# Optimization experiments

Hardware: AMD Instinct MI355X
Metric: run time of the kernel (lower is better)

The kernel has to match this reference:

```python
import jax, jax.numpy as jnp
import numpy as np

N, F, HID, H, B = 400000, 128, 32, 4, 2000

def setup_inputs() -> dict:
    key = jax.random.key(0)
    ks = jax.random.split(key, 8)
    atom_fea = jax.random.normal(ks[0], (N, F), dtype=jnp.float32)
    segment_ids = jnp.sort(jax.random.randint(ks[1], (N,), 0, B, dtype=jnp.int32))
    s = 0.05
    return {
        "atom_fea": atom_fea,
        "segment_ids": segment_ids,
        "num_crystals": B,
        "W1": jax.random.normal(ks[2], (F, HID), dtype=jnp.float32) * s,
        "b1": jnp.zeros((HID,), dtype=jnp.float32),
        "W2": jax.random.normal(ks[3], (HID, H), dtype=jnp.float32) * s,
        "b2": jnp.zeros((H,), dtype=jnp.float32),
        "Wp": jax.random.normal(ks[4], (H * F, F), dtype=jnp.float32) * s,
        "bp": jnp.zeros((F,), dtype=jnp.float32),
    }

def reference(atom_fea, segment_ids, num_crystals, W1, b1, W2, b2, Wp, bp):
    # key MLP: (N,F) -> (N,H) attention logits (dropout is eval no-op)
    logits = jax.nn.silu(atom_fea @ W1 + b1) @ W2 + b2  # (N,H)
    # segment softmax over atoms within each crystal, per head
    seg_max = jax.ops.segment_max(logits, segment_ids, num_segments=num_crystals)
    ex = jnp.exp(logits - seg_max[segment_ids])
    denom = jax.ops.segment_sum(ex, segment_ids, num_segments=num_crystals)
    w = ex / denom[segment_ids]  # (N,H)
    # per-head softmax-weighted segment sum of atom features -> (B,H,F)
    weighted = jax.ops.segment_sum(
        w[:, :, None] * atom_fea[:, None, :], segment_ids, num_segments=num_crystals
    )
    flat = weighted.reshape(num_crystals, -1)  # (B, H*F)
    return jax.nn.silu(flat @ Wp + bp)  # (B,F)
```

## Files before the change

### kernel.cpp

```cpp
#include <hip/hip_runtime.h>
#include <math.h>

#define F 128
#define HID 32
#define NH 4
#define WTILE 16
#define BTILE 64
#define ROWB 512
#define PJC 4

typedef __attribute__((ext_vector_type(8))) short bf16x8;
typedef __attribute__((ext_vector_type(4))) float f32x4;

__device__ __forceinline__ float silu_f(float x) {
    return x / (1.0f + __expf(-x));
}

__device__ __forceinline__ uint f2bf(float f) {
    union { float f; uint u; } v; v.f = f;
    uint r = v.u + 0x7fffu + ((v.u >> 16) & 1u);
    return r >> 16;
}

__device__ __forceinline__ uint cvtpk_bf16(float lo, float hi) {
    uint r;
    asm("v_cvt_pk_bf16_f32 %0, %1, %2" : "=v"(r) : "v"(lo), "v"(hi));
    return r;
}

__device__ __forceinline__ void gload_lds16(const void* g, void* l) {
    __builtin_amdgcn_global_load_lds(
        (const __attribute__((address_space(1))) void*)g,
        (__attribute__((address_space(3))) void*)l, 16, 0, 0);
}

__global__ void seg_starts_kernel(const int* __restrict__ seg, int* __restrict__ starts,
                                  int N, int B) {
    int i = blockIdx.x * blockDim.x + threadIdx.x;
    if (i >= N) return;
    int id = seg[i];
    if (i == 0) {
        for (int b = 0; b <= id; ++b) starts[b] = 0;
    } else {
        int prev = seg[i - 1];
        for (int b = prev + 1; b <= id; ++b) starts[b] = i;
    }
    if (i == N - 1) {
        for (int b = id + 1; b <= B; ++b) starts[b] = N;
    }
}

__global__ __launch_bounds__(256, 2) void fused11_kernel(
    const float* __restrict__ atom_fea, const int* __restrict__ starts,
    const float* __restrict__ W1, const float* __restrict__ b1,
    const float* __restrict__ W2, const float* __restrict__ b2,
    float* __restrict__ gWacc) {
    __shared__ float sBuf[NH][2][WTILE * F];
    __shared__ float sTW[NH][WTILE * NH];

    const int t = threadIdx.x;
    const int b = blockIdx.x;
    const int start = starts[b];
    const int end = starts[b + 1];
    const int wv = t >> 6;
    const int lane = t & 63;
    const int lg = lane >> 4;
    const int l15 = lane & 15;
    const int ch = lane & 3;
    const int co = lane >> 2;
    const int lrh = lane >> 5;
    const int lch = lane & 31;

    bf16x8 w1f[2][4];
    #pragma unroll
    for (int m0 = 0; m0 < 2; ++m0)
        #pragma unroll
        for (int kk = 0; kk < 4; ++kk) {
            bf16x8 fr;
            #pragma unroll
            for (int j = 0; j < 8; ++j)
                fr[j] = (short)f2bf(W1[(kk * 32 + lg * 8 + j) * HID + m0 * 16 + l15]);
            w1f[m0][kk] = fr;
        }
    float b1r[8], w2r[8][4];
    #pragma unroll
    for (int m0 = 0; m0 < 2; ++m0)
        #pragma unroll
        for (int r = 0; r < 4; ++r) {
            const int h = m0 * 16 + lg * 4 + r;
            b1r[m0 * 4 + r] = b1[h];
            #pragma unroll
            for (int j = 0; j < 4; ++j) w2r[m0 * 4 + r][j] = W2[h * NH + j];
        }
    const float b2r0 = b2[0], b2r1 = b2[1], b2r2 = b2[2], b2r3 = b2[3];

    float m0_ = -INFINITY, m1_ = -INFINITY, m2_ = -INFINITY, m3_ = -INFINITY;
    float s0_ = 0.0f, s1_ = 0.0f, s2_ = 0.0f, s3_ = 0.0f;
    float acc8[8] = {0, 0, 0, 0, 0, 0, 0, 0};

    const int nt = (end > start) ? (end - start + BTILE - 1) / BTILE : 0;
    const char* gb = (const char*)atom_fea;
    char* bufA = (char*)&sBuf[wv][0][0];
    char* bufB = (char*)&sBuf[wv][1][0];

    if (nt > 0) {
        #pragma unroll
        for (int i = 0; i < 8; ++i) {
            const int lr = 2 * i + lrh;
            int ga = start + wv * WTILE + lr; ga = (ga < end) ? ga : end - 1;
            gload_lds16(gb + (size_t)ga * ROWB + ((lch ^ (lr & 7)) << 4), bufA + i * 1024);
        }
    }
    asm volatile("s_waitcnt vmcnt(0)" ::: "memory");

    int pb = 0;
    for (int ti = 0; ti < nt; ++ti) {
        const int base = start + ti * BTILE;
        const int T = min(BTILE, end - base);
        const int Tw = min(T - wv * WTILE, WTILE);
        char* bufc = pb ? bufB : bufA;

        if (ti + 1 < nt) {
            char* bufn = pb ? bufA : bufB;
            const int nb = base + BTILE;
            #pragma unroll
            for (int i = 0; i < 8; ++i) {
                const int lr = 2 * i + lrh;
                int ga = nb + wv * WTILE + lr; ga = (ga < end) ? ga : end - 1;
                gload_lds16(gb + (size_t)ga * ROWB + ((lch ^ (lr & 7)) << 4), bufn + i * 1024);
            }
        }

        if (Tw > 0) {
            f32x4 a0, a1;
            #pragma unroll
            for (int r = 0; r < 4; ++r) { a0[r] = b1r[r]; a1[r] = b1r[4 + r]; }
            const char* rb = bufc + l15 * ROWB;
            const int rs = l15 & 7;
            #pragma unroll
            for (int kk = 0; kk < 4; ++kk) {
                const int c0 = kk * 8 + lg * 2;
                const float4 va = *(const float4*)(rb + ((c0 ^ rs) << 4));
                const float4 vb = *(const float4*)(rb + (((c0 + 1) ^ rs) << 4));
                union { bf16x8 v; uint u[4]; } fr;
                fr.u[0] = cvtpk_bf16(va.x, va.y);
                fr.u[1] = cvtpk_bf16(va.z, va.w);
                fr.u[2] = cvtpk_bf16(vb.x, vb.y);
                fr.u[3] = cvtpk_bf16(vb.z, vb.w);
                a0 = __builtin_amdgcn_mfma_f32_16x16x32_bf16(w1f[0][kk], fr.v, a0, 0, 0, 0);
                a1 = __builtin_amdgcn_mfma_f32_16x16x32_bf16(w1f[1][kk], fr.v, a1, 0, 0, 0);
            }
            float p0 = 0, p1 = 0, p2 = 0, p3 = 0;
            #pragma unroll
            for (int r = 0; r < 4; ++r) {
                const float sa = silu_f(a0[r]);
                const float sb = silu_f(a1[r]);
                p0 = fmaf(sa, w2r[r][0], fmaf(sb, w2r[4 + r][0], p0));
                p1 = fmaf(sa, w2r[r][1], fmaf(sb, w2r[4 + r][1], p1));
                p2 = fmaf(sa, w2r[r][2], fmaf(sb, w2r[4 + r][2], p2));
                p3 = fmaf(sa, w2r[r][3], fmaf(sb, w2r[4 + r][3], p3));
            }
            p0 += __shfl_xor(p0, 16); p0 += __shfl_xor(p0, 32);
            p1 += __shfl_xor(p1, 16); p1 += __shfl_xor(p1, 32);
            p2 += __shfl_xor(p2, 16); p2 += __shfl_xor(p2, 32);
            p3 += __shfl_xor(p3, 16); p3 += __shfl_xor(p3, 32);
            const bool valid = (l15 < Tw);
            const float v0 = valid ? p0 + b2r0 : -INFINITY;
            const float v1 = valid ? p1 + b2r1 : -INFINITY;
            const float v2 = valid ? p2 + b2r2 : -INFINITY;
            const float v3 = valid ? p3 + b2r3 : -INFINITY;

            const float dm = fmaxf(fmaxf(v0 - m0_, v1 - m1_), fmaxf(v2 - m2_, v3 - m3_));
            if (__any(dm > 8.0f)) {
                float t0 = v0, t1 = v1, t2 = v2, t3 = v3;
                #pragma unroll
                for (int d = 1; d < 16; d <<= 1) {
                    t0 = fmaxf(t0, __shfl_xor(t0, d));
                    t1 = fmaxf(t1, __shfl_xor(t1, d));
                    t2 = fmaxf(t2, __shfl_xor(t2, d));
                    t3 = fmaxf(t3, __shfl_xor(t3, d));
                }
                const float n0 = fmaxf(m0_, t0), n1 = fmaxf(m1_, t1);
                const float n2 = fmaxf(m2_, t2), n3 = fmaxf(m3_, t3);
                const float r0 = __expf(m0_ - n0), r1 = __expf(m1_ - n1);
                const float r2 = __expf(m2_ - n2), r3 = __expf(m3_ - n3);
                s0_ *= r0; s1_ *= r1; s2_ *= r2; s3_ *= r3;
                m0_ = n0; m1_ = n1; m2_ = n2; m3_ = n3;
                const float rsel = (ch & 1) ? ((ch & 2) ? r3 : r1)
                                            : ((ch & 2) ? r2 : r0);
                #pragma unroll
                for (int j = 0; j < 8; ++j) acc8[j] *= rsel;
            }
            const float e0 = valid ? __expf(v0 - m0_) : 0.0f;
            const float e1 = valid ? __expf(v1 - m1_) : 0.0f;
            const float e2 = valid ? __expf(v2 - m2_) : 0.0f;
            const float e3 = valid ? __expf(v3 - m3_) : 0.0f;
            s0_ += e0; s1_ += e1; s2_ += e2; s3_ += e3;
            if (lane < 16) *(float4*)&sTW[wv][lane * NH] = make_float4(e0, e1, e2, e3);

            #pragma unroll 8
            for (int a = 0; a < WTILE; ++a) {
                const float w = sTW[wv][a * NH + ch];
                const int sw = a & 7;
                const char* ra = bufc + a * ROWB;
                const float4 q0 = *(const float4*)(ra + (((2 * co) ^ sw) << 4));
                const float4 q1 = *(const float4*)(ra + (((2 * co + 1) ^ sw) << 4));
                acc8[0] = fmaf(w, q0.x, acc8[0]);
                acc8[1] = fmaf(w, q0.y, acc8[1]);
                acc8[2] = fmaf(w, q0.z, acc8[2]);
                acc8[3] = fmaf(w, q0.w, acc8[3]);
                acc8[4] = fmaf(w, q1.x, acc8[4]);
                acc8[5] = fmaf(w, q1.y, acc8[5]);
                acc8[6] = fmaf(w, q1.z, acc8[6]);
                acc8[7] = fmaf(w, q1.w, acc8[7]);
            }
        }
        asm volatile("s_waitcnt vmcnt(0)" ::: "memory");
        pb ^= 1;
    }

    #pragma unroll
    for (int d = 1; d < 64; d <<= 1) {
        s0_ += __shfl_xor(s0_, d); s1_ += __shfl_xor(s1_, d);
        s2_ += __shfl_xor(s2_, d); s3_ += __shfl_xor(s3_, d);
    }
    float* epi = &sBuf[wv][0][0];
    *(float4*)&epi[lane * 8] = make_float4(acc8[0], acc8[1], acc8[2], acc8[3]);
    *(float4*)&epi[lane * 8 + 4] = make_float4(acc8[4], acc8[5], acc8[6], acc8[7]);
    if (lane == 0) {
        epi[512] = m0_; epi[513] = m1_; epi[514] = m2_; epi[515] = m3_;
        epi[516] = s0_ * 0.25f; epi[517] = s1_ * 0.25f;
        epi[518] = s2_ * 0.25f; epi[519] = s3_ * 0.25f;
    }
    __syncthreads();
    if (t < 64) {
        const int ch2 = t & 3, co2 = t >> 2;
        float mw[NH], fw[NH];
        float mg = -INFINITY;
        #pragma unroll
        for (int w = 0; w < NH; ++w) {
            mw[w] = sBuf[w][0][512 + ch2];
            mg = fmaxf(mg, mw[w]);
        }
        float sg = 0.0f;
        #pragma unroll
        for (int w = 0; w < NH; ++w) {
            fw[w] = (mw[w] == -INFINITY) ? 0.0f : __expf(mw[w] - mg);
            sg += sBuf[w][0][516 + ch2] * fw[w];
        }
        const float inv = (sg > 0.0f) ? 1.0f / sg : 0.0f;
        float o[8] = {0, 0, 0, 0, 0, 0, 0, 0};
        #pragma unroll
        for (int w = 0; w < NH; ++w) {
            const float* ap = &sBuf[w][0][t * 8];
            #pragma unroll
            for (int j = 0; j < 8; ++j) o[j] = fmaf(ap[j], fw[w], o[j]);
        }
        float* dst = &gWacc[(size_t)b * 512 + ch2 * F + co2 * 8];
        *(float4*)dst = make_float4(o[0] * inv, o[1] * inv, o[2] * inv, o[3] * inv);
        *(float4*)(dst + 4) = make_float4(o[4] * inv, o[5] * inv, o[6] * inv, o[7] * inv);
    }
}

__global__ __launch_bounds__(256) void proj_kernel(
    const float* __restrict__ gWacc, const float* __restrict__ Wp,
    const float* __restrict__ bp, float* __restrict__ out, int B) {
    __shared__ float sW[PJC * 512];
    __shared__ float sP[256 * PJC];
    const int t = threadIdx.x;
    const int c0 = blockIdx.x * PJC;
    for (int q = t; q < PJC * 512; q += 256) {
        const int cr = c0 + (q >> 9);
        sW[q] = (cr < B) ? gWacc[(size_t)cr * 512 + (q & 511)] : 0.0f;
    }
    __syncthreads();
    const int f = t & 127, half = t >> 7;
    float acc[PJC] = {};
    const float* wp = Wp + (size_t)(half * 256) * F + f;
    for (int k0 = 0; k0 < 256; k0 += 8) {
        float wpv[8];
        #pragma unroll
        for (int u = 0; u < 8; ++u) wpv[u] = wp[(size_t)(k0 + u) * F];
        #pragma unroll
        for (int u = 0; u < 8; ++u) {
            const int ks = half * 256 + k0 + u;
            #pragma unroll
            for (int g = 0; g < PJC; ++g) acc[g] = fmaf(sW[g * 512 + ks], wpv[u], acc[g]);
        }
    }
    #pragma unroll
    for (int g = 0; g < PJC; ++g) sP[t * PJC + g] = acc[g];
    __syncthreads();
    if (t < 128) {
        const float bpf = bp[t];
        #pragma unroll
        for (int g = 0; g < PJC; ++g) {
            const int cr = c0 + g;
            if (cr < B)
                out[(size_t)cr * F + t] =
                    silu_f(sP[t * PJC + g] + sP[(t + 128) * PJC + g] + bpf);
        }
    }
}

extern "C" void kernel_launch(void* const* d_in, const int* in_sizes, int n_in,
                              void* d_out, int out_size, void* d_ws, size_t ws_size,
                              hipStream_t stream) {
    const float* atom_fea = (const float*)d_in[0];
    const int* seg = (const int*)d_in[1];
    const float* W1 = (const float*)d_in[3];
    const float* b1 = (const float*)d_in[4];
    const float* W2 = (const float*)d_in[5];
    const float* b2 = (const float*)d_in[6];
    const float* Wp = (const float*)d_in[7];
    const float* bp = (const float*)d_in[8];
    float* out = (float*)d_out;

    const int N = in_sizes[0] / F;
    const int B = out_size / F;

    char* ws = (char*)d_ws;
    int* starts = (int*)ws;
    size_t off = (((size_t)(B + 1) * sizeof(int)) + 255) & ~(size_t)255;
    float* gWacc = (float*)(ws + off);

    seg_starts_kernel<<<(N + 255) / 256, 256, 0, stream>>>(seg, starts, N, B);
    fused11_kernel<<<B, 256, 0, stream>>>(atom_fea, starts, W1, b1, W2, b2, gWacc);
    proj_kernel<<<(B + PJC - 1) / PJC, 256, 0, stream>>>(gWacc, Wp, bp, out, B);
}
```

Baseline: 70.38 us.

## Drop LDS double-buffering and read atom rows directly from global memory

Removes the async global-to-LDS double-buffered staging of atom feature tiles. Each wave now independently walks 16-row chunks, strided across waves, and loads its rows straight from global memory twice: once for the MLP logits and once for the weighted accumulation. The second read is expected to hit in cache. This cuts LDS usage from about 64KB to about 9KB and removes the per-tile waitcnt synchronization, which should raise occupancy. The cost is losing explicit prefetch overlap and relying on L1/L2 for the reload.

```diff
diff --git a/kernel.cpp b/kernel.cpp
--- a/kernel.cpp
+++ b/kernel.cpp
@@ -5,7 +5,6 @@
 #define HID 32
 #define NH 4
 #define WTILE 16
-#define BTILE 64
 #define ROWB 512
 #define PJC 4
 
@@ -26,12 +25,6 @@
     uint r;
     asm("v_cvt_pk_bf16_f32 %0, %1, %2" : "=v"(r) : "v"(lo), "v"(hi));
     return r;
-}
-
-__device__ __forceinline__ void gload_lds16(const void* g, void* l) {
-    __builtin_amdgcn_global_load_lds(
-        (const __attribute__((address_space(1))) void*)g,
-        (__attribute__((address_space(3))) void*)l, 16, 0, 0);
 }
 
 __global__ void seg_starts_kernel(const int* __restrict__ seg, int* __restrict__ starts,
@@ -50,13 +43,13 @@
     }
 }
 
-__global__ __launch_bounds__(256, 2) void fused11_kernel(
+__global__ __launch_bounds__(256, 2) void fused12_kernel(
     const float* __restrict__ atom_fea, const int* __restrict__ starts,
     const float* __restrict__ W1, const float* __restrict__ b1,
     const float* __restrict__ W2, const float* __restrict__ b2,
     float* __restrict__ gWacc) {
-    __shared__ float sBuf[NH][2][WTILE * F];
     __shared__ float sTW[NH][WTILE * NH];
+    __shared__ float sEpi[NH][520];
 
     const int t = threadIdx.x;
     const int b = blockIdx.x;
@@ -68,8 +61,6 @@
     const int l15 = lane & 15;
     const int ch = lane & 3;
     const int co = lane >> 2;
-    const int lrh = lane >> 5;
-    const int lch = lane & 31;
 
     bf16x8 w1f[2][4];
     #pragma unroll
@@ -98,125 +89,99 @@
     float s0_ = 0.0f, s1_ = 0.0f, s2_ = 0.0f, s3_ = 0.0f;
     float acc8[8] = {0, 0, 0, 0, 0, 0, 0, 0};
 
-    const int nt = (end > start) ? (end - start + BTILE - 1) / BTILE : 0;
+    const int nc = (end > start) ? (end - start + WTILE - 1) / WTILE : 0;
     const char* gb = (const char*)atom_fea;
-    char* bufA = (char*)&sBuf[wv][0][0];
-    char* bufB = (char*)&sBuf[wv][1][0];
-
-    if (nt > 0) {
-        #pragma unroll
-        for (int i = 0; i < 8; ++i) {
-            const int lr = 2 * i + lrh;
-            int ga = start + wv * WTILE + lr; ga = (ga < end) ? ga : end - 1;
-            gload_lds16(gb + (size_t)ga * ROWB + ((lch ^ (lr & 7)) << 4), bufA + i * 1024);
-        }
-    }
-    asm volatile("s_waitcnt vmcnt(0)" ::: "memory");
-
-    int pb = 0;
-    for (int ti = 0; ti < nt; ++ti) {
-        const int base = start + ti * BTILE;
-        const int T = min(BTILE, end - base);
-        const int Tw = min(T - wv * WTILE, WTILE);
-        char* bufc = pb ? bufB : bufA;
-
-        if (ti + 1 < nt) {
-            char* bufn = pb ? bufA : bufB;
-            const int nb = base + BTILE;
-            #pragma unroll
-            for (int i = 0; i < 8; ++i) {
-                const int lr = 2 * i + lrh;
-                int ga = nb + wv * WTILE + lr; ga = (ga < end) ? ga : end - 1;
-                gload_lds16(gb + (size_t)ga * ROWB + ((lch ^ (lr & 7)) << 4), bufn + i * 1024);
+
+    for (int c = wv; c < nc; c += NH) {
+        const int abase = start + c * WTILE;
+        const int Tw = min(end - abase, WTILE);
+
+        int brow = abase + l15; brow = (brow < end) ? brow : end - 1;
+        const char* rb = gb + (size_t)brow * ROWB;
+        float4 va[4], vb[4];
+        #pragma unroll
+        for (int kk = 0; kk < 4; ++kk) {
+            va[kk] = *(const float4*)(rb + kk * 128 + lg * 32);
+            vb[kk] = *(const float4*)(rb + kk * 128 + lg * 32 + 16);
+        }
+        f32x4 a0, a1;
+        #pragma unroll
+        for (int r = 0; r < 4; ++r) { a0[r] = b1r[r]; a1[r] = b1r[4 + r]; }
+        #pragma unroll
+        for (int kk = 0; kk < 4; ++kk) {
+            union { bf16x8 v; uint u[4]; } fr;
+            fr.u[0] = cvtpk_bf16(va[kk].x, va[kk].y);
+            fr.u[1] = cvtpk_bf16(va[kk].z, va[kk].w);
+            fr.u[2] = cvtpk_bf16(vb[kk].x, vb[kk].y);
+            fr.u[3] = cvtpk_bf16(vb[kk].z, vb[kk].w);
+            a0 = __builtin_amdgcn_mfma_f32_16x16x32_bf16(w1f[0][kk], fr.v, a0, 0, 0, 0);
+            a1 = __builtin_amdgcn_mfma_f32_16x16x32_bf16(w1f[1][kk], fr.v, a1, 0, 0, 0);
+        }
+
+        float p0 = 0, p1 = 0, p2 = 0, p3 = 0;
+        #pragma unroll
+        for (int r = 0; r < 4; ++r) {
+            const float sa = silu_f(a0[r]);
+            const float sb = silu_f(a1[r]);
+            p0 = fmaf(sa, w2r[r][0], fmaf(sb, w2r[4 + r][0], p0));
+            p1 = fmaf(sa, w2r[r][1], fmaf(sb, w2r[4 + r][1], p1));
+            p2 = fmaf(sa, w2r[r][2], fmaf(sb, w2r[4 + r][2], p2));
+            p3 = fmaf(sa, w2r[r][3], fmaf(sb, w2r[4 + r][3], p3));
+        }
+        p0 += __shfl_xor(p0, 16); p0 += __shfl_xor(p0, 32);
+        p1 += __shfl_xor(p1, 16); p1 += __shfl_xor(p1, 32);
+        p2 += __shfl_xor(p2, 16); p2 += __shfl_xor(p2, 32);
+        p3 += __shfl_xor(p3, 16); p3 += __shfl_xor(p3, 32);
+        const bool valid = (l15 < Tw);
+        const float v0 = valid ? p0 + b2r0 : -INFINITY;
+        const float v1 = valid ? p1 + b2r1 : -INFINITY;
+        const float v2 = valid ? p2 + b2r2 : -INFINITY;
+        const float v3 = valid ? p3 + b2r3 : -INFINITY;
+
+        const float dm = fmaxf(fmaxf(v0 - m0_, v1 - m1_), fmaxf(v2 - m2_, v3 - m3_));
+        if (__any(dm > 8.0f)) {
+            float t0 = v0, t1 = v1, t2 = v2, t3 = v3;
+            #pragma unroll
+            for (int d = 1; d < 16; d <<= 1) {
+                t0 = fmaxf(t0, __shfl_xor(t0, d));
+                t1 = fmaxf(t1, __shfl_xor(t1, d));
+                t2 = fmaxf(t2, __shfl_xor(t2, d));
+                t3 = fmaxf(t3, __shfl_xor(t3, d));
             }
-        }
-
-        if (Tw > 0) {
-            f32x4 a0, a1;
-            #pragma unroll
-            for (int r = 0; r < 4; ++r) { a0[r] = b1r[r]; a1[r] = b1r[4 + r]; }
-            const char* rb = bufc + l15 * ROWB;
-            const int rs = l15 & 7;
-            #pragma unroll
-            for (int kk = 0; kk < 4; ++kk) {
-                const int c0 = kk * 8 + lg * 2;
-                const float4 va = *(const float4*)(rb + ((c0 ^ rs) << 4));
-                const float4 vb = *(const float4*)(rb + (((c0 + 1) ^ rs) << 4));
-                union { bf16x8 v; uint u[4]; } fr;
-                fr.u[0] = cvtpk_bf16(va.x, va.y);
-                fr.u[1] = cvtpk_bf16(va.z, va.w);
-                fr.u[2] = cvtpk_bf16(vb.x, vb.y);
-                fr.u[3] = cvtpk_bf16(vb.z, vb.w);
-                a0 = __builtin_amdgcn_mfma_f32_16x16x32_bf16(w1f[0][kk], fr.v, a0, 0, 0, 0);
-                a1 = __builtin_amdgcn_mfma_f32_16x16x32_bf16(w1f[1][kk], fr.v, a1, 0, 0, 0);
-            }
-            float p0 = 0, p1 = 0, p2 = 0, p3 = 0;
-            #pragma unroll
-            for (int r = 0; r < 4; ++r) {
-                const float sa = silu_f(a0[r]);
-                const float sb = silu_f(a1[r]);
-                p0 = fmaf(sa, w2r[r][0], fmaf(sb, w2r[4 + r][0], p0));
-                p1 = fmaf(sa, w2r[r][1], fmaf(sb, w2r[4 + r][1], p1));
-                p2 = fmaf(sa, w2r[r][2], fmaf(sb, w2r[4 + r][2], p2));
-                p3 = fmaf(sa, w2r[r][3], fmaf(sb, w2r[4 + r][3], p3));
-            }
-            p0 += __shfl_xor(p0, 16); p0 += __shfl_xor(p0, 32);
-            p1 += __shfl_xor(p1, 16); p1 += __shfl_xor(p1, 32);
-            p2 += __shfl_xor(p2, 16); p2 += __shfl_xor(p2, 32);
-            p3 += __shfl_xor(p3, 16); p3 += __shfl_xor(p3, 32);
-            const bool valid = (l15 < Tw);
-            const float v0 = valid ? p0 + b2r0 : -INFINITY;
-            const float v1 = valid ? p1 + b2r1 : -INFINITY;
-            const float v2 = valid ? p2 + b2r2 : -INFINITY;
-            const float v3 = valid ? p3 + b2r3 : -INFINITY;
-
-            const float dm = fmaxf(fmaxf(v0 - m0_, v1 - m1_), fmaxf(v2 - m2_, v3 - m3_));
-            if (__any(dm > 8.0f)) {
-                float t0 = v0, t1 = v1, t2 = v2, t3 = v3;
-                #pragma unroll
-                for (int d = 1; d < 16; d <<= 1) {
-                    t0 = fmaxf(t0, __shfl_xor(t0, d));
-                    t1 = fmaxf(t1, __shfl_xor(t1, d));
-                    t2 = fmaxf(t2, __shfl_xor(t2, d));
-                    t3 = fmaxf(t3, __shfl_xor(t3, d));
-                }
-                const float n0 = fmaxf(m0_, t0), n1 = fmaxf(m1_, t1);
-                const float n2 = fmaxf(m2_, t2), n3 = fmaxf(m3_, t3);
-                const float r0 = __expf(m0_ - n0), r1 = __expf(m1_ - n1);
-                const float r2 = __expf(m2_ - n2), r3 = __expf(m3_ - n3);
-                s0_ *= r0; s1_ *= r1; s2_ *= r2; s3_ *= r3;
-                m0_ = n0; m1_ = n1; m2_ = n2; m3_ = n3;
-                const float rsel = (ch & 1) ? ((ch & 2) ? r3 : r1)
-                                            : ((ch & 2) ? r2 : r0);
-                #pragma unroll
-                for (int j = 0; j < 8; ++j) acc8[j] *= rsel;
-            }
-            const float e0 = valid ? __expf(v0 - m0_) : 0.0f;
-            const float e1 = valid ? __expf(v1 - m1_) : 0.0f;
-            const float e2 = valid ? __expf(v2 - m2_) : 0.0f;
-            const float e3 = valid ? __expf(v3 - m3_) : 0.0f;
-            s0_ += e0; s1_ += e1; s2_ += e2; s3_ += e3;
-            if (lane < 16) *(float4*)&sTW[wv][lane * NH] = make_float4(e0, e1, e2, e3);
-
-            #pragma unroll 8
-            for (int a = 0; a < WTILE; ++a) {
-                const float w = sTW[wv][a * NH + ch];
-                const int sw = a & 7;
-                const char* ra = bufc + a * ROWB;
-                const float4 q0 = *(const float4*)(ra + (((2 * co) ^ sw) << 4));
-                const float4 q1 = *(const float4*)(ra + (((2 * co + 1) ^ sw) << 4));
-                acc8[0] = fmaf(w, q0.x, acc8[0]);
-                acc8[1] = fmaf(w, q0.y, acc8[1]);
-                acc8[2] = fmaf(w, q0.z, acc8[2]);
-                acc8[3] = fmaf(w, q0.w, acc8[3]);
-                acc8[4] = fmaf(w, q1.x, acc8[4]);
-                acc8[5] = fmaf(w, q1.y, acc8[5]);
-                acc8[6] = fmaf(w, q1.z, acc8[6]);
-                acc8[7] = fmaf(w, q1.w, acc8[7]);
-            }
-        }
-        asm volatile("s_waitcnt vmcnt(0)" ::: "memory");
-        pb ^= 1;
+            const float n0 = fmaxf(m0_, t0), n1 = fmaxf(m1_, t1);
+            const float n2 = fmaxf(m2_, t2), n3 = fmaxf(m3_, t3);
+            const float r0 = __expf(m0_ - n0), r1 = __expf(m1_ - n1);
+            const float r2 = __expf(m2_ - n2), r3 = __expf(m3_ - n3);
+            s0_ *= r0; s1_ *= r1; s2_ *= r2; s3_ *= r3;
+            m0_ = n0; m1_ = n1; m2_ = n2; m3_ = n3;
+            const float rsel = (ch & 1) ? ((ch & 2) ? r3 : r1)
+                                        : ((ch & 2) ? r2 : r0);
+            #pragma unroll
+            for (int j = 0; j < 8; ++j) acc8[j] *= rsel;
+        }
+        const float e0 = valid ? __expf(v0 - m0_) : 0.0f;
+        const float e1 = valid ? __expf(v1 - m1_) : 0.0f;
+        const float e2 = valid ? __expf(v2 - m2_) : 0.0f;
+        const float e3 = valid ? __expf(v3 - m3_) : 0.0f;
+        s0_ += e0; s1_ += e1; s2_ += e2; s3_ += e3;
+        if (lane < 16) *(float4*)&sTW[wv][lane * NH] = make_float4(e0, e1, e2, e3);
+
+        #pragma unroll 4
+        for (int a = 0; a < WTILE; ++a) {
+            const float w = sTW[wv][a * NH + ch];
+            int arow = abase + a; arow = (arow < end) ? arow : end - 1;
+            const char* ra = gb + (size_t)arow * ROWB;
+            const float4 q0 = *(const float4*)(ra + co * 32);
+            const float4 q1 = *(const float4*)(ra + co * 32 + 16);
+            acc8[0] = fmaf(w, q0.x, acc8[0]);
+            acc8[1] = fmaf(w, q0.y, acc8[1]);
+            acc8[2] = fmaf(w, q0.z, acc8[2]);
+            acc8[3] = fmaf(w, q0.w, acc8[3]);
+            acc8[4] = fmaf(w, q1.x, acc8[4]);
+            acc8[5] = fmaf(w, q1.y, acc8[5]);
+            acc8[6] = fmaf(w, q1.z, acc8[6]);
+            acc8[7] = fmaf(w, q1.w, acc8[7]);
+        }
     }
 
     #pragma unroll
@@ -224,13 +189,13 @@
         s0_ += __shfl_xor(s0_, d); s1_ += __shfl_xor(s1_, d);
         s2_ += __shfl_xor(s2_, d); s3_ += __shfl_xor(s3_, d);
     }
-    float* epi = &sBuf[wv][0][0];
-    *(float4*)&epi[lane * 8] = make_float4(acc8[0], acc8[1], acc8[2], acc8[3]);
-    *(float4*)&epi[lane * 8 + 4] = make_float4(acc8[4], acc8[5], acc8[6], acc8[7]);
+    *(float4*)&sEpi[wv][lane * 8] = make_float4(acc8[0], acc8[1], acc8[2], acc8[3]);
+    *(float4*)&sEpi[wv][lane * 8 + 4] = make_float4(acc8[4], acc8[5], acc8[6], acc8[7]);
     if (lane == 0) {
-        epi[512] = m0_; epi[513] = m1_; epi[514] = m2_; epi[515] = m3_;
-        epi[516] = s0_ * 0.25f; epi[517] = s1_ * 0.25f;
-        epi[518] = s2_ * 0.25f; epi[519] = s3_ * 0.25f;
+        sEpi[wv][512] = m0_; sEpi[wv][513] = m1_;
+        sEpi[wv][514] = m2_; sEpi[wv][515] = m3_;
+        sEpi[wv][516] = s0_ * 0.25f; sEpi[wv][517] = s1_ * 0.25f;
+        sEpi[wv][518] = s2_ * 0.25f; sEpi[wv][519] = s3_ * 0.25f;
     }
     __syncthreads();
     if (t < 64) {
@@ -239,20 +204,20 @@
         float mg = -INFINITY;
         #pragma unroll
         for (int w = 0; w < NH; ++w) {
-            mw[w] = sBuf[w][0][512 + ch2];
+            mw[w] = sEpi[w][512 + ch2];
             mg = fmaxf(mg, mw[w]);
         }
         float sg = 0.0f;
         #pragma unroll
         for (int w = 0; w < NH; ++w) {
             fw[w] = (mw[w] == -INFINITY) ? 0.0f : __expf(mw[w] - mg);
-            sg += sBuf[w][0][516 + ch2] * fw[w];
+            sg += sEpi[w][516 + ch2] * fw[w];
         }
         const float inv = (sg > 0.0f) ? 1.0f / sg : 0.0f;
         float o[8] = {0, 0, 0, 0, 0, 0, 0, 0};
         #pragma unroll
         for (int w = 0; w < NH; ++w) {
-            const float* ap = &sBuf[w][0][t * 8];
+            const float* ap = &sEpi[w][t * 8];
             #pragma unroll
             for (int j = 0; j < 8; ++j) o[j] = fmaf(ap[j], fw[w], o[j]);
         }
@@ -325,6 +290,6 @@
     float* gWacc = (float*)(ws + off);
 
     seg_starts_kernel<<<(N + 255) / 256, 256, 0, stream>>>(seg, starts, N, B);
-    fused11_kernel<<<B, 256, 0, stream>>>(atom_fea, starts, W1, b1, W2, b2, gWacc);
+    fused12_kernel<<<B, 256, 0, stream>>>(atom_fea, starts, W1, b1, W2, b2, gWacc);
     proj_kernel<<<(B + PJC - 1) / PJC, 256, 0, stream>>>(gWacc, Wp, bp, out, B);
 }
```

New measurement: 87.88 us. 24.9% more time.
